# Optimization experiments

Measured on AMD Instinct MI355X. Metric: run time of the kernel, lower is better.

Reference implementation:

```python
import jax, jax.numpy as jnp
import numpy as np

L, C, B = 256, 20, 1024


def _pos_mask(L):
    # pairwise mask: l2 - l1 >= 1, shape (L, L); broadcast over channels
    ls = jnp.arange(L)
    return (ls[None, :] - ls[:, None]) >= 1


def setup_inputs() -> dict:
    key = jax.random.key(0)
    k0, k1, k2 = jax.random.split(key, 3)
    x_lc = jax.random.uniform(k0, (B, L, C), dtype=jnp.float32)
    theta_0 = jnp.zeros((1,), dtype=jnp.float32)
    theta_lc = jax.random.normal(k1, (1, L, C), dtype=jnp.float32) / np.sqrt(L)
    pm = _pos_mask(L)
    theta_lclc = (jax.random.normal(k2, (1, L, C, L, C), dtype=jnp.float32)
                  / np.sqrt(L * L)) * pm[None, :, None, :, None]
    mask = pm
    return {"x_lc": x_lc, "theta_0": theta_0, "theta_lc": theta_lc,
            "theta_lclc": theta_lclc, "mask": mask}


def reference(x_lc, theta_0, theta_lc, theta_lclc, mask):
    Bn = x_lc.shape[0]
    # additive term: sum_{l,c} theta_lc * x
    phi = theta_0 + jnp.einsum('blc,zlc->b', x_lc, theta_lc)[:, None]
    # pairwise term as a masked bilinear form: x^T (mask * theta) x
    # (avoids materializing the (B,L,C,L,C) broadcast of the original)
    theta_m = theta_lclc[0] * mask[:, None, :, None].astype(theta_lclc.dtype)
    LC = L * C
    xf = x_lc.reshape(Bn, LC)                      # (B, LC)
    tf_ = theta_m.reshape(LC, LC)                  # (LC, LC)
    pair = jnp.einsum('bi,ij,bj->b', xf, tf_, xf)  # two GEMMs under the hood
    phi = phi + pair[:, None]
    return phi
```

## Files before the change

### kernel.cpp

```cpp
#include <hip/hip_runtime.h>
#include <stdint.h>

#define LDIM 256
#define CDIM 20
#define LC   5120
#define NB   1024
#define BM   128
#define BN   256
#define ITOT64 1640

typedef __attribute__((ext_vector_type(8))) short short8;
typedef __attribute__((ext_vector_type(4))) float float4v;
typedef __attribute__((ext_vector_type(4))) unsigned int uint4v;
typedef unsigned short ushort_t;

#define XB_BYTES (10485760ull)
#define WS_NEED  (XB_BYTES)

__device__ inline uint32_t pack_bf16x2(float a, float b) {
    uint32_t ua = __float_as_uint(a);
    uint32_t ub = __float_as_uint(b);
    ua += 0x7fffu + ((ua >> 16) & 1u);
    ub += 0x7fffu + ((ub >> 16) & 1u);
    return (ua >> 16) | (ub & 0xffff0000u);
}

__device__ inline float bf16_to_f32(ushort_t u) {
    return __uint_as_float(((uint32_t)u) << 16);
}

__device__ inline void load_lds16(const void* g, void* l) {
    __builtin_amdgcn_global_load_lds(
        (const __attribute__((address_space(1))) uint32_t*)g,
        (__attribute__((address_space(3))) uint32_t*)l, 16, 0, 0);
}

__global__ __launch_bounds__(256) void xconv_kernel(
    const float* __restrict__ X, const float* __restrict__ th0,
    const float* __restrict__ thlc, ushort_t* __restrict__ Xb,
    float* __restrict__ out)
{
    const int b = blockIdx.x;
    const int t = threadIdx.x;
    __shared__ float red[4];

    const float*  src = X  + (size_t)b * LC;
    ushort_t*     dst = Xb + (size_t)b * LC;
    float s = 0.f;
    for (int c = t * 4; c < LC; c += 1024) {
        float4 f = *(const float4*)(src + c);
        float4 w = *(const float4*)(thlc + c);
        s += f.x * w.x + f.y * w.y + f.z * w.z + f.w * w.w;
        uint2 u;
        u.x = pack_bf16x2(f.x, f.y);
        u.y = pack_bf16x2(f.z, f.w);
        *(uint2*)(dst + c) = u;
    }
    s += __shfl_xor(s, 1);  s += __shfl_xor(s, 2);  s += __shfl_xor(s, 4);
    s += __shfl_xor(s, 8);  s += __shfl_xor(s, 16); s += __shfl_xor(s, 32);
    if ((t & 63) == 0) red[t >> 6] = s;
    __syncthreads();
    if (t == 0) out[b] = th0[0] + red[0] + red[1] + red[2] + red[3];
}

__global__ __launch_bounds__(256, 2) void pair_fused(
    const float* __restrict__ T, const ushort_t* __restrict__ Xb,
    float* __restrict__ out)
{
    const int n    = blockIdx.x;
    const int kblk = ((n >> 3) << 1) | (n & 1);
    const int bn0  = ((n >> 1) & 3) * BN;

    const int gbeg = (ITOT64 * kblk) >> 7;
    const int gend = (ITOT64 * (kblk + 1)) >> 7;

    int it = 0, pre = 0;
    while (pre + (80 - 2 * it) <= gbeg) { pre += 80 - 2 * it; ++it; }
    int li = gbeg - pre;

    __shared__ __align__(16) ushort_t A_s[1024 * 8];
    __shared__ __align__(16) ushort_t B_s[2][2048 * 8];

    const int t    = threadIdx.x;
    const int lane = t & 63;
    const int wid  = t >> 6;
    const int wm   = (wid >> 1) * 64;
    const int wn   = (wid & 1) * 128;
    const int l16  = lane & 15;
    const int qk   = lane >> 4;

    const int r32 = t >> 3;
    const int ga  = t & 7;
    uint32_t offTa[4];
    int      wAdr[4];
    #pragma unroll
    for (int j = 0; j < 4; ++j) {
        const int row = r32 + j * 32;
        offTa[j] = (uint32_t)row * LC + (ga << 3);
        wAdr[j]  = ((row << 3) + (ga ^ (row & 7))) << 4;
    }

    uint32_t offB[8];
    #pragma unroll
    for (int j = 0; j < 8; ++j) {
        const int c = (wid << 9) + (j << 6) + lane;
        const int row = c >> 3;
        const int g2 = (c & 7) ^ (row & 7);
        offB[j] = (uint32_t)(bn0 + row) * LC + (g2 << 3);
    }

    int adrA[2][4], adrB[2][8];
    #pragma unroll
    for (int step = 0; step < 2; ++step) {
        const int kf = step * 4 + qk;
        #pragma unroll
        for (int mt = 0; mt < 4; ++mt) {
            const int r = wm + mt * 16 + l16;
            adrA[step][mt] = ((r << 3) + (kf ^ (r & 7))) << 4;
        }
        #pragma unroll
        for (int nt = 0; nt < 8; ++nt) {
            const int r = wn + nt * 16 + l16;
            adrB[step][nt] = ((r << 3) + (kf ^ (r & 7))) << 4;
        }
    }

    int i0 = it << 7;
    int k0 = i0 + (li << 6);

    float4v acc[4][8];
    #pragma unroll
    for (int mt = 0; mt < 4; ++mt)
        #pragma unroll
        for (int nt = 0; nt < 8; ++nt)
            #pragma unroll
            for (int r = 0; r < 4; ++r) acc[mt][nt][r] = 0.f;

    {
        const float* Tb0 = T + (size_t)i0 * LC + k0;
        float4 p0[4], p1[4];
        #pragma unroll
        for (int j = 0; j < 4; ++j) {
            p0[j] = *(const float4*)(Tb0 + offTa[j]);
            p1[j] = *(const float4*)(Tb0 + offTa[j] + 4);
        }
        #pragma unroll
        for (int j = 0; j < 8; ++j)
            load_lds16(Xb + k0 + offB[j], &B_s[0][(((wid << 9) + (j << 6)) << 3)]);
        #pragma unroll
        for (int j = 0; j < 4; ++j) {
            uint4v v;
            v[0] = pack_bf16x2(p0[j].x, p0[j].y);
            v[1] = pack_bf16x2(p0[j].z, p0[j].w);
            v[2] = pack_bf16x2(p1[j].x, p1[j].y);
            v[3] = pack_bf16x2(p1[j].z, p1[j].w);
            *(uint4v*)((char*)A_s + wAdr[j]) = v;
        }
    }

    int cur = 0;
    float4 a0[4], a1[4];

    for (int g = gbeg; g < gend; ++g) {
        const bool haveNext = (g + 1 < gend);
        const int  li_n   = li + 1;
        const bool segEnd = (li_n == 80 - 2 * it);
        const int  it_n   = segEnd ? it + 1 : it;
        const int  i0_n   = it_n << 7;
        const int  k0_n   = segEnd ? i0_n : (k0 + 64);

        if (haveNext) {
            const float* Tb2 = T + (size_t)i0_n * LC + k0_n;
            #pragma unroll
            for (int j = 0; j < 4; ++j) {
                a0[j] = *(const float4*)(Tb2 + offTa[j]);
                a1[j] = *(const float4*)(Tb2 + offTa[j] + 4);
            }
            #pragma unroll
            for (int j = 0; j < 8; ++j)
                load_lds16(Xb + k0_n + offB[j],
                           &B_s[cur ^ 1][(((wid << 9) + (j << 6)) << 3)]);
        }
        __builtin_amdgcn_sched_barrier(0);
        if (haveNext)
            asm volatile("s_waitcnt vmcnt(16) lgkmcnt(0)" ::: "memory");
        else
            asm volatile("s_waitcnt vmcnt(0) lgkmcnt(0)" ::: "memory");
        __builtin_amdgcn_s_barrier();
        __builtin_amdgcn_sched_barrier(0);

        const char* Bbase = (const char*)B_s[cur];
        #pragma unroll
        for (int step = 0; step < 2; ++step) {
            short8 af[4], bfr[8];
            #pragma unroll
            for (int mt = 0; mt < 4; ++mt)
                af[mt] = *(const short8*)((const char*)A_s + adrA[step][mt]);
            #pragma unroll
            for (int nt = 0; nt < 8; ++nt)
                bfr[nt] = *(const short8*)(Bbase + adrB[step][nt]);
            __builtin_amdgcn_s_setprio(1);
            #pragma unroll
            for (int mt = 0; mt < 4; ++mt)
                #pragma unroll
                for (int nt = 0; nt < 8; ++nt)
                    acc[mt][nt] = __builtin_amdgcn_mfma_f32_16x16x32_bf16(
                        af[mt], bfr[nt], acc[mt][nt], 0, 0, 0);
            __builtin_amdgcn_s_setprio(0);
        }

        __builtin_amdgcn_sched_barrier(0);
        __builtin_amdgcn_s_barrier();
        __builtin_amdgcn_sched_barrier(0);

        if (haveNext) {
            #pragma unroll
            for (int j = 0; j < 4; ++j) {
                uint4v v;
                v[0] = pack_bf16x2(a0[j].x, a0[j].y);
                v[1] = pack_bf16x2(a0[j].z, a0[j].w);
                v[2] = pack_bf16x2(a1[j].x, a1[j].y);
                v[3] = pack_bf16x2(a1[j].z, a1[j].w);
                *(uint4v*)((char*)A_s + wAdr[j]) = v;
            }
        }

        if (segEnd || !haveNext) {
            #pragma unroll
            for (int nt = 0; nt < 8; ++nt) {
                const int b = bn0 + wn + nt * 16 + l16;
                const ushort_t* xb = Xb + (size_t)b * LC + i0 + wm + qk * 4;
                float s = 0.f;
                #pragma unroll
                for (int mt = 0; mt < 4; ++mt) {
                    ushort4 xv = *(const ushort4*)(xb + mt * 16);
                    s += acc[mt][nt][0] * bf16_to_f32(xv.x)
                       + acc[mt][nt][1] * bf16_to_f32(xv.y)
                       + acc[mt][nt][2] * bf16_to_f32(xv.z)
                       + acc[mt][nt][3] * bf16_to_f32(xv.w);
                }
                s += __shfl_xor(s, 16);
                s += __shfl_xor(s, 32);
                if (qk == 0) atomicAdd(&out[b], s);
            }
            #pragma unroll
            for (int mt = 0; mt < 4; ++mt)
                #pragma unroll
                for (int nt = 0; nt < 8; ++nt)
                    #pragma unroll
                    for (int r = 0; r < 4; ++r) acc[mt][nt][r] = 0.f;
        }

        li = segEnd ? 0 : li_n;
        it = it_n;
        i0 = i0_n;
        k0 = k0_n;
        cur ^= 1;
    }
}

__global__ __launch_bounds__(256) void init_kernel(
    const float* __restrict__ x, const float* __restrict__ th0,
    const float* __restrict__ thlc, float* __restrict__ out)
{
    const int b = blockIdx.x;
    const float4* xb = (const float4*)(x + (size_t)b * LC);
    const float4* tv = (const float4*)thlc;
    float s = 0.f;
    for (int i = threadIdx.x; i < LC / 4; i += 256) {
        float4 a = xb[i], t = tv[i];
        s += a.x * t.x + a.y * t.y + a.z * t.z + a.w * t.w;
    }
    s += __shfl_xor(s, 1);  s += __shfl_xor(s, 2);  s += __shfl_xor(s, 4);
    s += __shfl_xor(s, 8);  s += __shfl_xor(s, 16); s += __shfl_xor(s, 32);
    __shared__ float red[4];
    if ((threadIdx.x & 63) == 0) red[threadIdx.x >> 6] = s;
    __syncthreads();
    if (threadIdx.x == 0) out[b] = th0[0] + red[0] + red[1] + red[2] + red[3];
}

__global__ __launch_bounds__(256) void pair_kernel(
    const float* __restrict__ T, const float* __restrict__ X,
    float* __restrict__ out)
{
    const int n  = blockIdx.x;
    const int r  = n & 7;
    const int g  = n >> 3;
    const int i0  = (g >> 3) * BM;
    const int bn0 = (g & 7) * 128;
    const int kstart = i0;
    const int nIter  = (LC - kstart) >> 6;
    const int ipc    = (nIter + 7) >> 3;
    const int itBeg  = r * ipc;
    const int itEnd  = (itBeg + ipc < nIter) ? (itBeg + ipc) : nIter;
    if (itBeg >= itEnd) return;
    const int kbeg   = kstart + (itBeg << 6);

    __shared__ __align__(16) short A_s[8 * BM * 8];
    __shared__ __align__(16) short B_s[8 * BM * 8];

    const int t    = threadIdx.x;
    const int lane = t & 63;
    const int wid  = t >> 6;
    const int wm   = (wid >> 1) * 64;
    const int wn   = (wid & 1) * 64;
    const int l16  = lane & 15;
    const int qk   = lane >> 4;

    const float* pA[4]; const float* pB[4]; int sIdx[4];
    #pragma unroll
    for (int u = 0; u < 4; ++u) {
        const int id  = t + u * 256;
        const int row = id >> 3;
        const int kq  = id & 7;
        pA[u] = T + (size_t)(i0 + row) * LC + kbeg + kq * 8;
        pB[u] = X + (size_t)(bn0 + row) * LC + kbeg + kq * 8;
        sIdx[u] = (kq * BM + (row ^ kq)) * 8;
    }

    float4v acc[4][4] = {};
    for (int itr = itBeg; itr < itEnd; ++itr) {
        __syncthreads();
        #pragma unroll
        for (int u = 0; u < 4; ++u) {
            float4 a0 = ((const float4*)pA[u])[0];
            float4 a1 = ((const float4*)pA[u])[1];
            float4 b0 = ((const float4*)pB[u])[0];
            float4 b1 = ((const float4*)pB[u])[1];
            pA[u] += 64; pB[u] += 64;
            uint4v va, vb;
            va[0] = pack_bf16x2(a0.x, a0.y); va[1] = pack_bf16x2(a0.z, a0.w);
            va[2] = pack_bf16x2(a1.x, a1.y); va[3] = pack_bf16x2(a1.z, a1.w);
            vb[0] = pack_bf16x2(b0.x, b0.y); vb[1] = pack_bf16x2(b0.z, b0.w);
            vb[2] = pack_bf16x2(b1.x, b1.y); vb[3] = pack_bf16x2(b1.z, b1.w);
            *(uint4v*)(A_s + sIdx[u]) = va;
            *(uint4v*)(B_s + sIdx[u]) = vb;
        }
        __syncthreads();
        #pragma unroll
        for (int step = 0; step < 2; ++step) {
            const int kf = step * 4 + qk;
            short8 af[4], bfr[4];
            #pragma unroll
            for (int mt = 0; mt < 4; ++mt)
                af[mt] = *(const short8*)(A_s + (kf * BM + ((wm + mt * 16 + l16) ^ kf)) * 8);
            #pragma unroll
            for (int nt = 0; nt < 4; ++nt)
                bfr[nt] = *(const short8*)(B_s + (kf * BM + ((wn + nt * 16 + l16) ^ kf)) * 8);
            #pragma unroll
            for (int mt = 0; mt < 4; ++mt)
                #pragma unroll
                for (int nt = 0; nt < 4; ++nt)
                    acc[mt][nt] = __builtin_amdgcn_mfma_f32_16x16x32_bf16(
                        af[mt], bfr[nt], acc[mt][nt], 0, 0, 0);
        }
    }
    #pragma unroll
    for (int nt = 0; nt < 4; ++nt) {
        const int b = bn0 + wn + nt * 16 + l16;
        const float* xb = X + (size_t)b * LC + i0 + wm + qk * 4;
        float s = 0.f;
        #pragma unroll
        for (int mt = 0; mt < 4; ++mt) {
            float4 xv = *(const float4*)(xb + mt * 16);
            s += acc[mt][nt][0] * xv.x + acc[mt][nt][1] * xv.y +
                 acc[mt][nt][2] * xv.z + acc[mt][nt][3] * xv.w;
        }
        s += __shfl_xor(s, 16);
        s += __shfl_xor(s, 32);
        if (qk == 0) atomicAdd(&out[b], s);
    }
}

extern "C" void kernel_launch(void* const* d_in, const int* in_sizes, int n_in,
                              void* d_out, int out_size, void* d_ws, size_t ws_size,
                              hipStream_t stream) {
    const float* x    = (const float*)d_in[0];
    const float* th0  = (const float*)d_in[1];
    const float* thlc = (const float*)d_in[2];
    const float* T    = (const float*)d_in[3];
    float* out = (float*)d_out;

    if (ws_size >= WS_NEED) {
        ushort_t* Xb = (ushort_t*)d_ws;
        xconv_kernel<<<NB, 256, 0, stream>>>(x, th0, thlc, Xb, out);
        pair_fused<<<512, 256, 0, stream>>>(T, Xb, out);
    } else {
        init_kernel<<<NB, 256, 0, stream>>>(x, th0, thlc, out);
        pair_kernel<<<(LC / BM) * (NB / 128) * 8, 256, 0, stream>>>(T, x, out);
    }
}
```

Measured before the change: 251.8 us.

## Load T tile at iteration start instead of register-prefetching next tile

```diff
diff --git a/kernel.cpp b/kernel.cpp
--- a/kernel.cpp
+++ b/kernel.cpp
@@ -136,30 +136,11 @@
             #pragma unroll
             for (int r = 0; r < 4; ++r) acc[mt][nt][r] = 0.f;
 
-    {
-        const float* Tb0 = T + (size_t)i0 * LC + k0;
-        float4 p0[4], p1[4];
-        #pragma unroll
-        for (int j = 0; j < 4; ++j) {
-            p0[j] = *(const float4*)(Tb0 + offTa[j]);
-            p1[j] = *(const float4*)(Tb0 + offTa[j] + 4);
-        }
-        #pragma unroll
-        for (int j = 0; j < 8; ++j)
-            load_lds16(Xb + k0 + offB[j], &B_s[0][(((wid << 9) + (j << 6)) << 3)]);
-        #pragma unroll
-        for (int j = 0; j < 4; ++j) {
-            uint4v v;
-            v[0] = pack_bf16x2(p0[j].x, p0[j].y);
-            v[1] = pack_bf16x2(p0[j].z, p0[j].w);
-            v[2] = pack_bf16x2(p1[j].x, p1[j].y);
-            v[3] = pack_bf16x2(p1[j].z, p1[j].w);
-            *(uint4v*)((char*)A_s + wAdr[j]) = v;
-        }
-    }
+    #pragma unroll
+    for (int j = 0; j < 8; ++j)
+        load_lds16(Xb + k0 + offB[j], &B_s[0][(((wid << 9) + (j << 6)) << 3)]);
 
     int cur = 0;
-    float4 a0[4], a1[4];
 
     for (int g = gbeg; g < gend; ++g) {
         const bool haveNext = (g + 1 < gend);
@@ -169,23 +150,37 @@
         const int  i0_n   = it_n << 7;
         const int  k0_n   = segEnd ? i0_n : (k0 + 64);
 
+        const float* Tbase = T + (size_t)i0 * LC + k0;
+        float4 a0[4], a1[4];
+        #pragma unroll
+        for (int j = 0; j < 4; ++j) {
+            a0[j] = *(const float4*)(Tbase + offTa[j]);
+            a1[j] = *(const float4*)(Tbase + offTa[j] + 4);
+        }
+
+        __builtin_amdgcn_sched_barrier(0);
+        __builtin_amdgcn_s_barrier();
+        __builtin_amdgcn_sched_barrier(0);
+
         if (haveNext) {
-            const float* Tb2 = T + (size_t)i0_n * LC + k0_n;
-            #pragma unroll
-            for (int j = 0; j < 4; ++j) {
-                a0[j] = *(const float4*)(Tb2 + offTa[j]);
-                a1[j] = *(const float4*)(Tb2 + offTa[j] + 4);
-            }
             #pragma unroll
             for (int j = 0; j < 8; ++j)
                 load_lds16(Xb + k0_n + offB[j],
                            &B_s[cur ^ 1][(((wid << 9) + (j << 6)) << 3)]);
         }
+
+        #pragma unroll
+        for (int j = 0; j < 4; ++j) {
+            uint4v v;
+            v[0] = pack_bf16x2(a0[j].x, a0[j].y);
+            v[1] = pack_bf16x2(a0[j].z, a0[j].w);
+            v[2] = pack_bf16x2(a1[j].x, a1[j].y);
+            v[3] = pack_bf16x2(a1[j].z, a1[j].w);
+            *(uint4v*)((char*)A_s + wAdr[j]) = v;
+        }
+
+        asm volatile("s_waitcnt lgkmcnt(0)" ::: "memory");
         __builtin_amdgcn_sched_barrier(0);
-        if (haveNext)
-            asm volatile("s_waitcnt vmcnt(16) lgkmcnt(0)" ::: "memory");
-        else
-            asm volatile("s_waitcnt vmcnt(0) lgkmcnt(0)" ::: "memory");
         __builtin_amdgcn_s_barrier();
         __builtin_amdgcn_sched_barrier(0);
 
@@ -207,22 +202,6 @@
                     acc[mt][nt] = __builtin_amdgcn_mfma_f32_16x16x32_bf16(
                         af[mt], bfr[nt], acc[mt][nt], 0, 0, 0);
             __builtin_amdgcn_s_setprio(0);
-        }
-
-        __builtin_amdgcn_sched_barrier(0);
-        __builtin_amdgcn_s_barrier();
-        __builtin_amdgcn_sched_barrier(0);
-
-        if (haveNext) {
-            #pragma unroll
-            for (int j = 0; j < 4; ++j) {
-                uint4v v;
-                v[0] = pack_bf16x2(a0[j].x, a0[j].y);
-                v[1] = pack_bf16x2(a0[j].z, a0[j].w);
-                v[2] = pack_bf16x2(a1[j].x, a1[j].y);
-                v[3] = pack_bf16x2(a1[j].z, a1[j].w);
-                *(uint4v*)((char*)A_s + wAdr[j]) = v;
-            }
         }
 
         if (segEnd || !haveNext) {
```

Measured after the change: 210.4 us. -16.4%, faster.
